# Kernel tuning notes

Measured on AMD Instinct MI355X. Metric: run time of the kernel, lower is better.

Reference implementation:

```python
import jax, jax.numpy as jnp
import numpy as np

N = 100000   # nodes
E = 1250000  # directed edges
F = 32       # node_features
H = 64       # hidden_channels
C = 10       # num_classes
NEG_SLOPE = 0.2  # GATConv default LeakyReLU slope


def _glorot(key, shape):
    fan_in = shape[0]
    return jax.random.normal(key, shape, jnp.float32) / np.sqrt(fan_in)


def setup_inputs() -> dict:
    k = jax.random.split(jax.random.key(0), 16)
    x = jax.random.normal(k[0], (N, F), jnp.float32)
    edge_index = jax.random.randint(k[1], (2, E), 0, N, dtype=jnp.int32)
    return {
        "x": x,
        "edge_index": edge_index,
        # GCNConv 1
        "W1": _glorot(k[2], (F, H)), "b1": jnp.zeros((H,), jnp.float32),
        # GATConv (heads=1)
        "W2": _glorot(k[3], (H, H)),
        "a_src": _glorot(k[4], (H,)), "a_dst": _glorot(k[5], (H,)),
        "b2": jnp.zeros((H,), jnp.float32),
        # GCNConv 3
        "W3": _glorot(k[6], (H, H)), "b3": jnp.zeros((H,), jnp.float32),
        # optimization head
        "Wopt": _glorot(k[7], (H, C)), "bopt": jnp.zeros((C,), jnp.float32),
        # bottleneck detector MLP
        "Wb1": _glorot(k[8], (H, 32)), "bb1": jnp.zeros((32,), jnp.float32),
        "Wb2": _glorot(k[9], (32, 1)), "bb2": jnp.zeros((1,), jnp.float32),
    }


def _gcn_conv(x, W, b, src, dst, n):
    # PyG GCNConv: self-loops already appended to src/dst by caller.
    h = x @ W  # [n, out]
    deg = jnp.zeros((n,), x.dtype).at[dst].add(1.0)
    dinv = jax.lax.rsqrt(jnp.maximum(deg, 1e-12))
    norm = dinv[src] * dinv[dst]  # [e]
    msg = h[src] * norm[:, None]  # gather + scale
    out = jnp.zeros_like(h).at[dst].add(msg)  # scatter-add
    return out + b


def _gat_conv(x, W, a_src, a_dst, b, src, dst, n):
    # PyG GATConv, heads=1: self-loops already appended.
    h = x @ W  # [n, out]
    alpha_s = h @ a_src  # [n]
    alpha_d = h @ a_dst  # [n]
    e = jax.nn.leaky_relu(alpha_s[src] + alpha_d[dst], NEG_SLOPE)  # [e]
    # softmax over incoming edges of each dst node
    emax = jax.ops.segment_max(e, dst, num_segments=n)
    p = jnp.exp(e - emax[dst])
    denom = jax.ops.segment_sum(p, dst, num_segments=n)
    alpha = p / denom[dst]
    out = jnp.zeros_like(h).at[dst].add(h[src] * alpha[:, None])
    return out + b


def reference(x, edge_index, W1, b1, W2, a_src, a_dst, b2, W3, b3,
              Wopt, bopt, Wb1, bb1, Wb2, bb2):
    n = x.shape[0]
    loops = jnp.arange(n, dtype=edge_index.dtype)
    src = jnp.concatenate([edge_index[0], loops])
    dst = jnp.concatenate([edge_index[1], loops])

    h = jax.nn.relu(_gcn_conv(x, W1, b1, src, dst, n))
    h = jax.nn.relu(_gat_conv(h, W2, a_src, a_dst, b2, src, dst, n))
    h = jax.nn.relu(_gcn_conv(h, W3, b3, src, dst, n))

    optimizations = h @ Wopt + bopt                     # [n, C]
    bottlenecks = jax.nn.sigmoid(jax.nn.relu(h @ Wb1 + bb1) @ Wb2 + bb2)  # [n, 1]
    graph_embedding = h.mean(axis=0)                    # [H]
    return optimizations, bottlenecks, graph_embedding
```

## Files before the change

### kernel.cpp

```cpp
#include <hip/hip_runtime.h>
#include <hip/hip_bf16.h>


#define CAP 64
#define NP2 128
#define NB2MAX 800

__device__ __forceinline__ int uwave(){
  return __builtin_amdgcn_readfirstlane(threadIdx.x >> 6);
}
__device__ __forceinline__ unsigned short f2bf(float f){
  unsigned u = __float_as_uint(f);
  return (unsigned short)((u + 0x7fffu + ((u >> 16) & 1u)) >> 16);
}
__device__ __forceinline__ float bfl(unsigned u){ return __uint_as_float(u << 16); }
__device__ __forceinline__ float bfh(unsigned u){ return __uint_as_float(u & 0xffff0000u); }
__device__ __forceinline__ float rdlane(float v, int l){
  return __uint_as_float(__builtin_amdgcn_readlane(__float_as_uint(v), l));
}

__global__ void k_setup(const float* __restrict__ Wopt, const float* __restrict__ bopt,
                        const float* __restrict__ Wb1, const float* __restrict__ bb1,
                        float* __restrict__ Wcat, float* __restrict__ bcat,
                        int* __restrict__ bcnt, unsigned short* __restrict__ tb,
                        unsigned short* __restrict__ xh, float* __restrict__ emb_acc,
                        int n, int nb2){
  int i = blockIdx.x*blockDim.x + threadIdx.x;
  if (i < nb2) bcnt[i] = 0;
  if (blockIdx.x == 0){
    int tid = threadIdx.x;
    for (int j = tid; j < 4096; j += 256){
      int f = j >> 6, c = j & 63;
      float w = 0.f;
      if (c < 10)       w = Wopt[f*10 + c];
      else if (c >= 32) w = Wb1[f*32 + (c-32)];
      Wcat[j] = w;
    }
    if (tid < 64){
      float b = 0.f;
      if (tid < 10)       b = bopt[tid];
      else if (tid >= 32) b = bb1[tid-32];
      bcat[tid] = b;
      tb[(size_t)n*64 + tid] = 0;
      emb_acc[tid] = 0.f;
    }
    if (tid >= 64 && tid < 96) xh[(size_t)n*32 + (tid-64)] = 0;
  }
}

__global__ __launch_bounds__(256) void k_part(const int* __restrict__ src,
                        const int* __restrict__ dst,
                        uint2* __restrict__ pairs, int* __restrict__ bcnt,
                        int e, int nb2, int pbcap){
  __shared__ int lcnt[NB2MAX];
  __shared__ int lbase[NB2MAX];
  int tid = threadIdx.x;
  for (int j = tid; j < nb2; j += 256) lcnt[j] = 0;
  __syncthreads();
  int i0 = blockIdx.x*2048 + tid*8;
  int d[8], s[8], bk[8], lp[8];
  int nv = e - i0;
  if (nv > 8) nv = 8;
  if (nv < 0) nv = 0;
  if (nv == 8){
    int4 d0 = *(const int4*)(dst + i0), d1 = *(const int4*)(dst + i0 + 4);
    int4 s0 = *(const int4*)(src + i0), s1 = *(const int4*)(src + i0 + 4);
    d[0]=d0.x; d[1]=d0.y; d[2]=d0.z; d[3]=d0.w;
    d[4]=d1.x; d[5]=d1.y; d[6]=d1.z; d[7]=d1.w;
    s[0]=s0.x; s[1]=s0.y; s[2]=s0.z; s[3]=s0.w;
    s[4]=s1.x; s[5]=s1.y; s[6]=s1.z; s[7]=s1.w;
  } else {
    #pragma unroll
    for (int j = 0; j < 8; j++){ d[j] = 0; s[j] = 0; }
    for (int j = 0; j < nv; j++){ d[j] = dst[i0+j]; s[j] = src[i0+j]; }
  }
  #pragma unroll
  for (int j = 0; j < 8; j++){
    if (j < nv){
      bk[j] = d[j] >> 7;
      lp[j] = atomicAdd(&lcnt[bk[j]], 1);
    }
  }
  __syncthreads();
  for (int j = tid; j < nb2; j += 256){
    int c = lcnt[j];
    if (c) lbase[j] = atomicAdd(&bcnt[j], c);
  }
  __syncthreads();
  #pragma unroll
  for (int j = 0; j < 8; j++){
    if (j < nv){
      int p = lbase[bk[j]] + lp[j];
      if (p < pbcap)
        pairs[(size_t)bk[j]*pbcap + p] = make_uint2((unsigned)d[j], (unsigned)s[j]);
    }
  }
}

__global__ __launch_bounds__(256) void k_fill(const uint2* __restrict__ pairs,
                        const int* __restrict__ bcnt, int* __restrict__ cnt,
                        int* __restrict__ adj, int pbcap, int n){
  __shared__ int lc[NP2];
  __shared__ int ladj[NP2*CAP];
  int b = blockIdx.x;
  int lo = b << 7;
  int nn = min(NP2, n - lo);
  int tid = threadIdx.x;
  for (int j = tid; j < NP2; j += 256) lc[j] = 0;
  __syncthreads();
  int m = bcnt[b];
  if (m > pbcap) m = pbcap;
  const uint2* pb = pairs + (size_t)b*pbcap;
  for (int j = tid; j < m; j += 256){
    uint2 p = pb[j];
    int r = (int)p.x - lo;
    int pos = atomicAdd(&lc[r], 1);
    if (pos < CAP) ladj[(r << 6) + pos] = (int)p.y;
  }
  __syncthreads();
  if (tid < nn) cnt[lo + tid] = lc[tid];
  int tot = nn << 4;
  uint4* ga = (uint4*)(adj + (size_t)lo*CAP);
  const uint4* la = (const uint4*)ladj;
  for (int j = tid; j < tot; j += 256) ga[j] = la[j];
}

__global__ void k_castscale(const float* __restrict__ x, const int* __restrict__ cnt,
                            unsigned short* __restrict__ xh, int total4){
  int i = blockIdx.x*blockDim.x + threadIdx.x;
  if (i >= total4) return;
  int row = i >> 3;
  float dv = rsqrtf((float)(cnt[row] + 1));
  float4 v = ((const float4*)x)[i];
  uint2 o;
  o.x = (unsigned)f2bf(v.x*dv) | ((unsigned)f2bf(v.y*dv) << 16);
  o.y = (unsigned)f2bf(v.z*dv) | ((unsigned)f2bf(v.w*dv) << 16);
  ((uint2*)xh)[i] = o;
}

__global__ __launch_bounds__(256) void k_agg32g(const unsigned short* __restrict__ xh,
                          const int* __restrict__ adj, const int* __restrict__ cnt,
                          const float* __restrict__ W1, const float* __restrict__ b1,
                          unsigned short* __restrict__ h, int n){
  int lane = threadIdx.x & 63;
  float wreg[32];
  #pragma unroll
  for (int k = 0; k < 32; k++) wreg[k] = W1[k*64 + lane];
  float br = b1[lane];
  int v0 = blockIdx.x*8 + uwave()*2;
  if (v0 >= n) return;
  int v1 = v0 + 1;
  bool has1 = v1 < n;
  if (!has1) v1 = v0;
  int cn0 = cnt[v0], cn1 = cnt[v1];
  int c0 = min(cn0, CAP), c1 = min(cn1, CAP);
  int ureg0 = n, ureg1 = n;
  if (lane < c0) ureg0 = (adj + (size_t)v0*CAP)[lane];
  if (lane < c1) ureg1 = (adj + (size_t)v1*CAP)[lane];
  int g = lane >> 3, q = lane & 7;
  float4 a0 = {0.f,0.f,0.f,0.f}, a1 = {0.f,0.f,0.f,0.f};
  int itm = (max(c0, c1) + 7) >> 3;
  #pragma unroll 2
  for (int jj = 0; jj < itm; jj++){
    int u0 = __shfl(ureg0, jj*8 + g);
    int u1 = __shfl(ureg1, jj*8 + g);
    uint2 r0 = ((const uint2*)(xh + (size_t)u0*32))[q];
    uint2 r1 = ((const uint2*)(xh + (size_t)u1*32))[q];
    a0.x += bfl(r0.x); a0.y += bfh(r0.x); a0.z += bfl(r0.y); a0.w += bfh(r0.y);
    a1.x += bfl(r1.x); a1.y += bfh(r1.x); a1.z += bfl(r1.y); a1.w += bfh(r1.y);
  }
  #pragma unroll
  for (int off = 8; off <= 32; off <<= 1){
    a0.x += __shfl_xor(a0.x, off); a0.y += __shfl_xor(a0.y, off);
    a0.z += __shfl_xor(a0.z, off); a0.w += __shfl_xor(a0.w, off);
    a1.x += __shfl_xor(a1.x, off); a1.y += __shfl_xor(a1.y, off);
    a1.z += __shfl_xor(a1.z, off); a1.w += __shfl_xor(a1.w, off);
  }
  uint2 s0 = ((const uint2*)(xh + (size_t)v0*32))[q];
  uint2 s1 = ((const uint2*)(xh + (size_t)v1*32))[q];
  a0.x += bfl(s0.x); a0.y += bfh(s0.x); a0.z += bfl(s0.y); a0.w += bfh(s0.y);
  a1.x += bfl(s1.x); a1.y += bfh(s1.x); a1.z += bfl(s1.y); a1.w += bfh(s1.y);
  float dv0 = rsqrtf((float)(cn0 + 1)), dv1 = rsqrtf((float)(cn1 + 1));
  a0.x *= dv0; a0.y *= dv0; a0.z *= dv0; a0.w *= dv0;
  a1.x *= dv1; a1.y *= dv1; a1.z *= dv1; a1.w *= dv1;
  float h0 = br, h1v = br;
  #pragma unroll
  for (int q2 = 0; q2 < 8; q2++){
    float w0x = rdlane(a0.x, q2), w1x = rdlane(a1.x, q2);
    float w0y = rdlane(a0.y, q2), w1y = rdlane(a1.y, q2);
    float w0z = rdlane(a0.z, q2), w1z = rdlane(a1.z, q2);
    float w0w = rdlane(a0.w, q2), w1w = rdlane(a1.w, q2);
    h0 = fmaf(w0x, wreg[q2*4+0], h0); h1v = fmaf(w1x, wreg[q2*4+0], h1v);
    h0 = fmaf(w0y, wreg[q2*4+1], h0); h1v = fmaf(w1y, wreg[q2*4+1], h1v);
    h0 = fmaf(w0z, wreg[q2*4+2], h0); h1v = fmaf(w1z, wreg[q2*4+2], h1v);
    h0 = fmaf(w0w, wreg[q2*4+3], h0); h1v = fmaf(w1w, wreg[q2*4+3], h1v);
  }
  h[(size_t)v0*64 + lane] = f2bf(fmaxf(h0, 0.f));
  if (has1) h[(size_t)v1*64 + lane] = f2bf(fmaxf(h1v, 0.f));
}

template<bool SCALE>
__global__ __launch_bounds__(256, 4) void k_gemm_b(const unsigned short* __restrict__ x,
                       const float* __restrict__ W, const int* __restrict__ cnt,
                       unsigned short* __restrict__ t, int n){
  int lane = threadIdx.x & 63;
  int gw = blockIdx.x*4 + uwave();
  int nw = gridDim.x*4;
  float wreg[64];
  #pragma unroll
  for (int k = 0; k < 64; k++) wreg[k] = W[k*64 + lane];
  for (int v = gw; v < n; v += nw){
    const uint4* xr = (const uint4*)(x + (size_t)v*64);
    float acc = 0.f;
    #pragma unroll
    for (int k8 = 0; k8 < 8; k8++){
      uint4 c = xr[k8];
      acc = fmaf(bfl(c.x), wreg[k8*8+0], acc);
      acc = fmaf(bfh(c.x), wreg[k8*8+1], acc);
      acc = fmaf(bfl(c.y), wreg[k8*8+2], acc);
      acc = fmaf(bfh(c.y), wreg[k8*8+3], acc);
      acc = fmaf(bfl(c.z), wreg[k8*8+4], acc);
      acc = fmaf(bfh(c.z), wreg[k8*8+5], acc);
      acc = fmaf(bfl(c.w), wreg[k8*8+6], acc);
      acc = fmaf(bfh(c.w), wreg[k8*8+7], acc);
    }
    if (SCALE) acc *= rsqrtf((float)(cnt[v] + 1));
    t[(size_t)v*64 + lane] = f2bf(acc);
  }
}

__global__ __launch_bounds__(256, 4) void k_gemm_alpha(const unsigned short* __restrict__ x,
                       const float* __restrict__ W,
                       const float* __restrict__ asrc, const float* __restrict__ adst,
                       unsigned short* __restrict__ t, float* __restrict__ als,
                       float* __restrict__ ald, int n){
  int lane = threadIdx.x & 63;
  int gw = blockIdx.x*4 + uwave();
  int nw = gridDim.x*4;
  float wreg[64];
  #pragma unroll
  for (int k = 0; k < 64; k++) wreg[k] = W[k*64 + lane];
  float asr = asrc[lane], adr = adst[lane];
  for (int v = gw; v < n; v += nw){
    const uint4* xr = (const uint4*)(x + (size_t)v*64);
    float acc = 0.f;
    #pragma unroll
    for (int k8 = 0; k8 < 8; k8++){
      uint4 c = xr[k8];
      acc = fmaf(bfl(c.x), wreg[k8*8+0], acc);
      acc = fmaf(bfh(c.x), wreg[k8*8+1], acc);
      acc = fmaf(bfl(c.y), wreg[k8*8+2], acc);
      acc = fmaf(bfh(c.y), wreg[k8*8+3], acc);
      acc = fmaf(bfl(c.z), wreg[k8*8+4], acc);
      acc = fmaf(bfh(c.z), wreg[k8*8+5], acc);
      acc = fmaf(bfl(c.w), wreg[k8*8+6], acc);
      acc = fmaf(bfh(c.w), wreg[k8*8+7], acc);
    }
    t[(size_t)v*64 + lane] = f2bf(acc);
    float s1 = acc * asr, s2 = acc * adr;
    #pragma unroll
    for (int off = 32; off; off >>= 1){
      s1 += __shfl_xor(s1, off);
      s2 += __shfl_xor(s2, off);
    }
    if (lane == 0){ als[v] = s1; ald[v] = s2; }
  }
}

__global__ __launch_bounds__(256) void k_gcn_agg(const unsigned short* __restrict__ t,
                          const int* __restrict__ adj, const int* __restrict__ cnt,
                          const float* __restrict__ b, unsigned short* __restrict__ h, int n){
  int lane = threadIdx.x & 63;
  int v0 = blockIdx.x*8 + uwave()*2;
  if (v0 >= n) return;
  int v1 = v0 + 1;
  bool has1 = v1 < n;
  if (!has1) v1 = v0;
  int cn0 = cnt[v0], cn1 = cnt[v1];
  int c0 = min(cn0, CAP), c1 = min(cn1, CAP);
  int ureg0 = n, ureg1 = n;
  if (lane < c0) ureg0 = (adj + (size_t)v0*CAP)[lane];
  if (lane < c1) ureg1 = (adj + (size_t)v1*CAP)[lane];
  int g = lane >> 3, q = lane & 7;
  float a0[8] = {0,0,0,0,0,0,0,0}, a1[8] = {0,0,0,0,0,0,0,0};
  int itm = (max(c0, c1) + 7) >> 3;
  #pragma unroll 2
  for (int jj = 0; jj < itm; jj++){
    int u0 = __shfl(ureg0, jj*8 + g);
    int u1 = __shfl(ureg1, jj*8 + g);
    uint4 r0 = ((const uint4*)(t + (size_t)u0*64))[q];
    uint4 r1 = ((const uint4*)(t + (size_t)u1*64))[q];
    a0[0] += bfl(r0.x); a0[1] += bfh(r0.x); a0[2] += bfl(r0.y); a0[3] += bfh(r0.y);
    a0[4] += bfl(r0.z); a0[5] += bfh(r0.z); a0[6] += bfl(r0.w); a0[7] += bfh(r0.w);
    a1[0] += bfl(r1.x); a1[1] += bfh(r1.x); a1[2] += bfl(r1.y); a1[3] += bfh(r1.y);
    a1[4] += bfl(r1.z); a1[5] += bfh(r1.z); a1[6] += bfl(r1.w); a1[7] += bfh(r1.w);
  }
  #pragma unroll
  for (int off = 8; off <= 32; off <<= 1){
    #pragma unroll
    for (int k = 0; k < 8; k++){
      a0[k] += __shfl_xor(a0[k], off);
      a1[k] += __shfl_xor(a1[k], off);
    }
  }
  uint4 s0 = ((const uint4*)(t + (size_t)v0*64))[q];
  uint4 s1 = ((const uint4*)(t + (size_t)v1*64))[q];
  a0[0] += bfl(s0.x); a0[1] += bfh(s0.x); a0[2] += bfl(s0.y); a0[3] += bfh(s0.y);
  a0[4] += bfl(s0.z); a0[5] += bfh(s0.z); a0[6] += bfl(s0.w); a0[7] += bfh(s0.w);
  a1[0] += bfl(s1.x); a1[1] += bfh(s1.x); a1[2] += bfl(s1.y); a1[3] += bfh(s1.y);
  a1[4] += bfl(s1.z); a1[5] += bfh(s1.z); a1[6] += bfl(s1.w); a1[7] += bfh(s1.w);
  float dv0 = rsqrtf((float)(cn0 + 1)), dv1 = rsqrtf((float)(cn1 + 1));
  float4 b0 = ((const float4*)b)[2*q], b1v = ((const float4*)b)[2*q+1];
  if (g == 0){
    float r0 = fmaxf(fmaf(a0[0], dv0, b0.x), 0.f),  r1 = fmaxf(fmaf(a0[1], dv0, b0.y), 0.f);
    float r2 = fmaxf(fmaf(a0[2], dv0, b0.z), 0.f),  r3 = fmaxf(fmaf(a0[3], dv0, b0.w), 0.f);
    float r4 = fmaxf(fmaf(a0[4], dv0, b1v.x), 0.f), r5 = fmaxf(fmaf(a0[5], dv0, b1v.y), 0.f);
    float r6 = fmaxf(fmaf(a0[6], dv0, b1v.z), 0.f), r7 = fmaxf(fmaf(a0[7], dv0, b1v.w), 0.f);
    uint4 o;
    o.x = (unsigned)f2bf(r0) | ((unsigned)f2bf(r1) << 16);
    o.y = (unsigned)f2bf(r2) | ((unsigned)f2bf(r3) << 16);
    o.z = (unsigned)f2bf(r4) | ((unsigned)f2bf(r5) << 16);
    o.w = (unsigned)f2bf(r6) | ((unsigned)f2bf(r7) << 16);
    ((uint4*)(h + (size_t)v0*64))[q] = o;
  } else if (g == 1 && has1){
    float r0 = fmaxf(fmaf(a1[0], dv1, b0.x), 0.f),  r1 = fmaxf(fmaf(a1[1], dv1, b0.y), 0.f);
    float r2 = fmaxf(fmaf(a1[2], dv1, b0.z), 0.f),  r3 = fmaxf(fmaf(a1[3], dv1, b0.w), 0.f);
    float r4 = fmaxf(fmaf(a1[4], dv1, b1v.x), 0.f), r5 = fmaxf(fmaf(a1[5], dv1, b1v.y), 0.f);
    float r6 = fmaxf(fmaf(a1[6], dv1, b1v.z), 0.f), r7 = fmaxf(fmaf(a1[7], dv1, b1v.w), 0.f);
    uint4 o;
    o.x = (unsigned)f2bf(r0) | ((unsigned)f2bf(r1) << 16);
    o.y = (unsigned)f2bf(r2) | ((unsigned)f2bf(r3) << 16);
    o.z = (unsigned)f2bf(r4) | ((unsigned)f2bf(r5) << 16);
    o.w = (unsigned)f2bf(r6) | ((unsigned)f2bf(r7) << 16);
    ((uint4*)(h + (size_t)v1*64))[q] = o;
  }
}

__global__ __launch_bounds__(256) void k_gat_agg(const unsigned short* __restrict__ t,
                          const int* __restrict__ adj, const int* __restrict__ cnt,
                          const float* __restrict__ als, const float* __restrict__ ald,
                          const float* __restrict__ b, unsigned short* __restrict__ h, int n){
  int lane = threadIdx.x & 63;
  int v0 = blockIdx.x*8 + uwave()*2;
  if (v0 >= n) return;
  int v1 = v0 + 1;
  bool has1 = v1 < n;
  if (!has1) v1 = v0;
  int c0 = min(cnt[v0], CAP), c1 = min(cnt[v1], CAP);
  int ureg0 = n, ureg1 = n;
  if (lane < c0) ureg0 = (adj + (size_t)v0*CAP)[lane];
  if (lane < c1) ureg1 = (adj + (size_t)v1*CAP)[lane];
  int us0 = (lane < c0) ? ureg0 : v0;
  int us1 = (lane < c1) ? ureg1 : v1;
  float adv0 = ald[v0], adv1 = ald[v1];
  float e0 = als[us0] + adv0;
  float e1 = als[us1] + adv1;
  e0 = e0 > 0.f ? e0 : 0.2f*e0;
  e1 = e1 > 0.f ? e1 : 0.2f*e1;
  float es0 = als[v0] + adv0; es0 = es0 > 0.f ? es0 : 0.2f*es0;
  float es1 = als[v1] + adv1; es1 = es1 > 0.f ? es1 : 0.2f*es1;
  float em0 = (lane < c0) ? e0 : -1e30f;
  float em1 = (lane < c1) ? e1 : -1e30f;
  #pragma unroll
  for (int off = 32; off; off >>= 1){
    em0 = fmaxf(em0, __shfl_xor(em0, off));
    em1 = fmaxf(em1, __shfl_xor(em1, off));
  }
  em0 = fmaxf(em0, es0); em1 = fmaxf(em1, es1);
  float p0 = (lane < c0) ? __expf(e0 - em0) : 0.f;
  float p1 = (lane < c1) ? __expf(e1 - em1) : 0.f;
  float sm0 = p0, sm1 = p1;
  #pragma unroll
  for (int off = 32; off; off >>= 1){
    sm0 += __shfl_xor(sm0, off);
    sm1 += __shfl_xor(sm1, off);
  }
  float ps0 = __expf(es0 - em0), ps1 = __expf(es1 - em1);
  float inv0 = 1.f / (sm0 + ps0), inv1 = 1.f / (sm1 + ps1);
  int g = lane >> 3, q = lane & 7;
  float a0[8] = {0,0,0,0,0,0,0,0}, a1[8] = {0,0,0,0,0,0,0,0};
  int itm = (max(c0, c1) + 7) >> 3;
  #pragma unroll 2
  for (int jj = 0; jj < itm; jj++){
    int   u0 = __shfl(ureg0, jj*8 + g);
    int   u1 = __shfl(ureg1, jj*8 + g);
    float w0 = __shfl(p0,    jj*8 + g);
    float w1 = __shfl(p1,    jj*8 + g);
    uint4 r0 = ((const uint4*)(t + (size_t)u0*64))[q];
    uint4 r1 = ((const uint4*)(t + (size_t)u1*64))[q];
    a0[0] = fmaf(w0, bfl(r0.x), a0[0]); a0[1] = fmaf(w0, bfh(r0.x), a0[1]);
    a0[2] = fmaf(w0, bfl(r0.y), a0[2]); a0[3] = fmaf(w0, bfh(r0.y), a0[3]);
    a0[4] = fmaf(w0, bfl(r0.z), a0[4]); a0[5] = fmaf(w0, bfh(r0.z), a0[5]);
    a0[6] = fmaf(w0, bfl(r0.w), a0[6]); a0[7] = fmaf(w0, bfh(r0.w), a0[7]);
    a1[0] = fmaf(w1, bfl(r1.x), a1[0]); a1[1] = fmaf(w1, bfh(r1.x), a1[1]);
    a1[2] = fmaf(w1, bfl(r1.y), a1[2]); a1[3] = fmaf(w1, bfh(r1.y), a1[3]);
    a1[4] = fmaf(w1, bfl(r1.z), a1[4]); a1[5] = fmaf(w1, bfh(r1.z), a1[5]);
    a1[6] = fmaf(w1, bfl(r1.w), a1[6]); a1[7] = fmaf(w1, bfh(r1.w), a1[7]);
  }
  #pragma unroll
  for (int off = 8; off <= 32; off <<= 1){
    #pragma unroll
    for (int k = 0; k < 8; k++){
      a0[k] += __shfl_xor(a0[k], off);
      a1[k] += __shfl_xor(a1[k], off);
    }
  }
  uint4 s0 = ((const uint4*)(t + (size_t)v0*64))[q];
  uint4 s1 = ((const uint4*)(t + (size_t)v1*64))[q];
  a0[0] = fmaf(ps0, bfl(s0.x), a0[0]); a0[1] = fmaf(ps0, bfh(s0.x), a0[1]);
  a0[2] = fmaf(ps0, bfl(s0.y), a0[2]); a0[3] = fmaf(ps0, bfh(s0.y), a0[3]);
  a0[4] = fmaf(ps0, bfl(s0.z), a0[4]); a0[5] = fmaf(ps0, bfh(s0.z), a0[5]);
  a0[6] = fmaf(ps0, bfl(s0.w), a0[6]); a0[7] = fmaf(ps0, bfh(s0.w), a0[7]);
  a1[0] = fmaf(ps1, bfl(s1.x), a1[0]); a1[1] = fmaf(ps1, bfh(s1.x), a1[1]);
  a1[2] = fmaf(ps1, bfl(s1.y), a1[2]); a1[3] = fmaf(ps1, bfh(s1.y), a1[3]);
  a1[4] = fmaf(ps1, bfl(s1.z), a1[4]); a1[5] = fmaf(ps1, bfh(s1.z), a1[5]);
  a1[6] = fmaf(ps1, bfl(s1.w), a1[6]); a1[7] = fmaf(ps1, bfh(s1.w), a1[7]);
  float4 b0 = ((const float4*)b)[2*q], b1v = ((const float4*)b)[2*q+1];
  if (g == 0){
    float r0 = fmaxf(fmaf(a0[0], inv0, b0.x), 0.f),  r1 = fmaxf(fmaf(a0[1], inv0, b0.y), 0.f);
    float r2 = fmaxf(fmaf(a0[2], inv0, b0.z), 0.f),  r3 = fmaxf(fmaf(a0[3], inv0, b0.w), 0.f);
    float r4 = fmaxf(fmaf(a0[4], inv0, b1v.x), 0.f), r5 = fmaxf(fmaf(a0[5], inv0, b1v.y), 0.f);
    float r6 = fmaxf(fmaf(a0[6], inv0, b1v.z), 0.f), r7 = fmaxf(fmaf(a0[7], inv0, b1v.w), 0.f);
    uint4 o;
    o.x = (unsigned)f2bf(r0) | ((unsigned)f2bf(r1) << 16);
    o.y = (unsigned)f2bf(r2) | ((unsigned)f2bf(r3) << 16);
    o.z = (unsigned)f2bf(r4) | ((unsigned)f2bf(r5) << 16);
    o.w = (unsigned)f2bf(r6) | ((unsigned)f2bf(r7) << 16);
    ((uint4*)(h + (size_t)v0*64))[q] = o;
  } else if (g == 1 && has1){
    float r0 = fmaxf(fmaf(a1[0], inv1, b0.x), 0.f),  r1 = fmaxf(fmaf(a1[1], inv1, b0.y), 0.f);
    float r2 = fmaxf(fmaf(a1[2], inv1, b0.z), 0.f),  r3 = fmaxf(fmaf(a1[3], inv1, b0.w), 0.f);
    float r4 = fmaxf(fmaf(a1[4], inv1, b1v.x), 0.f), r5 = fmaxf(fmaf(a1[5], inv1, b1v.y), 0.f);
    float r6 = fmaxf(fmaf(a1[6], inv1, b1v.z), 0.f), r7 = fmaxf(fmaf(a1[7], inv1, b1v.w), 0.f);
    uint4 o;
    o.x = (unsigned)f2bf(r0) | ((unsigned)f2bf(r1) << 16);
    o.y = (unsigned)f2bf(r2) | ((unsigned)f2bf(r3) << 16);
    o.z = (unsigned)f2bf(r4) | ((unsigned)f2bf(r5) << 16);
    o.w = (unsigned)f2bf(r6) | ((unsigned)f2bf(r7) << 16);
    ((uint4*)(h + (size_t)v1*64))[q] = o;
  }
}

__global__ __launch_bounds__(256, 4) void k_heads(const unsigned short* __restrict__ h,
                        const float* __restrict__ Wcat, const float* __restrict__ bcat,
                        const float* __restrict__ Wb2, const float* __restrict__ bb2,
                        float* __restrict__ out_opt, float* __restrict__ out_bot, int n){
  int lane = threadIdx.x & 63;
  int gw = blockIdx.x*4 + uwave();
  int nw = gridDim.x*4;
  float wreg[64];
  #pragma unroll
  for (int k = 0; k < 64; k++) wreg[k] = Wcat[k*64 + lane];
  float bcr  = bcat[lane];
  float wb2r = (lane >= 32) ? Wb2[lane-32] : 0.f;
  float bb2r = bb2[0];
  for (int v = gw; v < n; v += nw){
    const uint4* xr = (const uint4*)(h + (size_t)v*64);
    float acc = bcr;
    #pragma unroll
    for (int k8 = 0; k8 < 8; k8++){
      uint4 c = xr[k8];
      acc = fmaf(bfl(c.x), wreg[k8*8+0], acc);
      acc = fmaf(bfh(c.x), wreg[k8*8+1], acc);
      acc = fmaf(bfl(c.y), wreg[k8*8+2], acc);
      acc = fmaf(bfh(c.y), wreg[k8*8+3], acc);
      acc = fmaf(bfl(c.z), wreg[k8*8+4], acc);
      acc = fmaf(bfh(c.z), wreg[k8*8+5], acc);
      acc = fmaf(bfl(c.w), wreg[k8*8+6], acc);
      acc = fmaf(bfh(c.w), wreg[k8*8+7], acc);
    }
    if (lane < 10) out_opt[(size_t)v*10 + lane] = acc;
    float contrib = fmaxf(acc, 0.f) * wb2r;
    #pragma unroll
    for (int off = 32; off; off >>= 1) contrib += __shfl_xor(contrib, off);
    if (lane == 0) out_bot[v] = 1.f / (1.f + __expf(-(contrib + bb2r)));
  }
}

__global__ __launch_bounds__(256) void k_mean(const unsigned short* __restrict__ h,
                       float* __restrict__ emb_acc, int n){
  __shared__ float red[256];
  int tid = threadIdx.x;
  int w = tid >> 6, lane = tid & 63;
  float s = 0.f;
  for (int r = blockIdx.x*4 + w; r < n; r += 1024)
    s += __uint_as_float(((unsigned)h[(size_t)r*64 + lane]) << 16);
  red[tid] = s;
  __syncthreads();
  if (tid < 64)
    atomicAdd(&emb_acc[tid], red[tid] + red[64+tid] + red[128+tid] + red[192+tid]);
}

__global__ void k_embed(const float* __restrict__ emb_acc, float* __restrict__ out_emb,
                        float invn){
  if (threadIdx.x < 64) out_emb[threadIdx.x] = emb_acc[threadIdx.x] * invn;
}

extern "C" void kernel_launch(void* const* d_in, const int* in_sizes, int n_in,
                              void* d_out, int out_size, void* d_ws, size_t ws_size,
                              hipStream_t stream) {
  const float* x    = (const float*)d_in[0];
  const int*   ei   = (const int*)d_in[1];
  const float* W1   = (const float*)d_in[2];
  const float* b1   = (const float*)d_in[3];
  const float* W2   = (const float*)d_in[4];
  const float* a_s  = (const float*)d_in[5];
  const float* a_d  = (const float*)d_in[6];
  const float* b2   = (const float*)d_in[7];
  const float* W3   = (const float*)d_in[8];
  const float* b3   = (const float*)d_in[9];
  const float* Wopt = (const float*)d_in[10];
  const float* bopt = (const float*)d_in[11];
  const float* Wb1  = (const float*)d_in[12];
  const float* bb1  = (const float*)d_in[13];
  const float* Wb2  = (const float*)d_in[14];
  const float* bb2  = (const float*)d_in[15];

  int n = in_sizes[0] / 32;
  int e = in_sizes[1] / 2;
  const int* src = ei;
  const int* dst = ei + e;

  char* ws = (char*)d_ws;
  size_t off = 0;
  auto alloc = [&](size_t bytes) -> void* {
    void* p = ws + off;
    off += (bytes + 255) & ~(size_t)255;
    return p;
  };
  int nb2 = (n + NP2 - 1) >> 7;
  int*            cnt     = (int*)           alloc((size_t)n * 4);
  int*            adj     = (int*)           alloc((size_t)n * CAP * 4);
  float*          als     = (float*)         alloc((size_t)n * 4);
  float*          ald     = (float*)         alloc((size_t)n * 4);
  unsigned short* xh      = (unsigned short*)alloc((size_t)(n+1) * 32 * 2);
  unsigned short* tb      = (unsigned short*)alloc((size_t)(n+1) * 64 * 2);
  unsigned short* hbuf    = (unsigned short*)alloc((size_t)n * 64 * 2);
  float*          emb_acc = (float*)         alloc((size_t)64 * 4);
  float*          Wcat    = (float*)         alloc((size_t)4096 * 4);
  float*          bcat    = (float*)         alloc((size_t)64 * 4);
  int*            bcnt    = (int*)           alloc((size_t)nb2 * 4);

  int pbcap = e / nb2 + 384;
  long pcap_max = ((long)n * 128) / ((long)nb2 * 8);
  if (pbcap > (int)pcap_max) pbcap = (int)pcap_max;
  uint2* pairs = (uint2*)hbuf;

  float* out_opt = (float*)d_out;
  float* out_bot = out_opt + (size_t)n * 10;
  float* out_emb = out_bot + n;

  int nb8    = (n + 7) / 8;
  int nbN    = (n + 255) / 256;
  int nbP    = (e + 2047) / 2048;
  int total4 = n*32/4;
  int nbC    = (total4 + 255) / 256;

  k_setup<<<nbN, 256, 0, stream>>>(Wopt, bopt, Wb1, bb1, Wcat, bcat,
                                   bcnt, tb, xh, emb_acc, n, nb2);
  k_part<<<nbP, 256, 0, stream>>>(src, dst, pairs, bcnt, e, nb2, pbcap);
  k_fill<<<nb2, 256, 0, stream>>>(pairs, bcnt, cnt, adj, pbcap, n);
  k_castscale<<<nbC, 256, 0, stream>>>(x, cnt, xh, total4);

  k_agg32g<<<nb8, 256, 0, stream>>>(xh, adj, cnt, W1, b1, hbuf, n);

  k_gemm_alpha<<<1024, 256, 0, stream>>>(hbuf, W2, a_s, a_d, tb, als, ald, n);
  k_gat_agg<<<nb8, 256, 0, stream>>>(tb, adj, cnt, als, ald, b2, hbuf, n);

  k_gemm_b<true><<<1024, 256, 0, stream>>>(hbuf, W3, cnt, tb, n);
  k_gcn_agg<<<nb8, 256, 0, stream>>>(tb, adj, cnt, b3, hbuf, n);

  k_heads<<<1024, 256, 0, stream>>>(hbuf, Wcat, bcat, Wb2, bb2,
                                    out_opt, out_bot, n);
  k_mean<<<256, 256, 0, stream>>>(hbuf, emb_acc, n);
  k_embed<<<1, 64, 0, stream>>>(emb_acc, out_emb, 1.0f / (float)n);
}
```

Baseline: 356.6 us.

## Switch GCN and GAT aggregation to one node per wave, one feature per lane

Both aggregation kernels are restructured so that each wavefront handles a single destination node, with each lane owning one of the 64 features. Neighbours are walked serially in an unroll-by-4 loop using scalar-style index loads. This removes the two-nodes-per-wave packing, the 8-way group split and the cross-lane shuffle reductions. In exchange, each gather issues a 2-byte load per lane (128 contiguous bytes per row) instead of 16-byte vector loads, the GAT kernel recomputes exp per edge in every lane, and the grid is doubled.

```diff
diff --git a/kernel.cpp b/kernel.cpp
--- a/kernel.cpp
+++ b/kernel.cpp
@@ -15,6 +15,7 @@
 }
 __device__ __forceinline__ float bfl(unsigned u){ return __uint_as_float(u << 16); }
 __device__ __forceinline__ float bfh(unsigned u){ return __uint_as_float(u & 0xffff0000u); }
+__device__ __forceinline__ float bfu(unsigned short s){ return __uint_as_float(((unsigned)s) << 16); }
 __device__ __forceinline__ float rdlane(float v, int l){
   return __uint_as_float(__builtin_amdgcn_readlane(__float_as_uint(v), l));
 }
@@ -271,69 +272,28 @@
                           const int* __restrict__ adj, const int* __restrict__ cnt,
                           const float* __restrict__ b, unsigned short* __restrict__ h, int n){
   int lane = threadIdx.x & 63;
-  int v0 = blockIdx.x*8 + uwave()*2;
-  if (v0 >= n) return;
-  int v1 = v0 + 1;
-  bool has1 = v1 < n;
-  if (!has1) v1 = v0;
-  int cn0 = cnt[v0], cn1 = cnt[v1];
-  int c0 = min(cn0, CAP), c1 = min(cn1, CAP);
-  int ureg0 = n, ureg1 = n;
-  if (lane < c0) ureg0 = (adj + (size_t)v0*CAP)[lane];
-  if (lane < c1) ureg1 = (adj + (size_t)v1*CAP)[lane];
-  int g = lane >> 3, q = lane & 7;
-  float a0[8] = {0,0,0,0,0,0,0,0}, a1[8] = {0,0,0,0,0,0,0,0};
-  int itm = (max(c0, c1) + 7) >> 3;
-  #pragma unroll 2
-  for (int jj = 0; jj < itm; jj++){
-    int u0 = __shfl(ureg0, jj*8 + g);
-    int u1 = __shfl(ureg1, jj*8 + g);
-    uint4 r0 = ((const uint4*)(t + (size_t)u0*64))[q];
-    uint4 r1 = ((const uint4*)(t + (size_t)u1*64))[q];
-    a0[0] += bfl(r0.x); a0[1] += bfh(r0.x); a0[2] += bfl(r0.y); a0[3] += bfh(r0.y);
-    a0[4] += bfl(r0.z); a0[5] += bfh(r0.z); a0[6] += bfl(r0.w); a0[7] += bfh(r0.w);
-    a1[0] += bfl(r1.x); a1[1] += bfh(r1.x); a1[2] += bfl(r1.y); a1[3] += bfh(r1.y);
-    a1[4] += bfl(r1.z); a1[5] += bfh(r1.z); a1[6] += bfl(r1.w); a1[7] += bfh(r1.w);
-  }
-  #pragma unroll
-  for (int off = 8; off <= 32; off <<= 1){
-    #pragma unroll
-    for (int k = 0; k < 8; k++){
-      a0[k] += __shfl_xor(a0[k], off);
-      a1[k] += __shfl_xor(a1[k], off);
-    }
-  }
-  uint4 s0 = ((const uint4*)(t + (size_t)v0*64))[q];
-  uint4 s1 = ((const uint4*)(t + (size_t)v1*64))[q];
-  a0[0] += bfl(s0.x); a0[1] += bfh(s0.x); a0[2] += bfl(s0.y); a0[3] += bfh(s0.y);
-  a0[4] += bfl(s0.z); a0[5] += bfh(s0.z); a0[6] += bfl(s0.w); a0[7] += bfh(s0.w);
-  a1[0] += bfl(s1.x); a1[1] += bfh(s1.x); a1[2] += bfl(s1.y); a1[3] += bfh(s1.y);
-  a1[4] += bfl(s1.z); a1[5] += bfh(s1.z); a1[6] += bfl(s1.w); a1[7] += bfh(s1.w);
-  float dv0 = rsqrtf((float)(cn0 + 1)), dv1 = rsqrtf((float)(cn1 + 1));
-  float4 b0 = ((const float4*)b)[2*q], b1v = ((const float4*)b)[2*q+1];
-  if (g == 0){
-    float r0 = fmaxf(fmaf(a0[0], dv0, b0.x), 0.f),  r1 = fmaxf(fmaf(a0[1], dv0, b0.y), 0.f);
-    float r2 = fmaxf(fmaf(a0[2], dv0, b0.z), 0.f),  r3 = fmaxf(fmaf(a0[3], dv0, b0.w), 0.f);
-    float r4 = fmaxf(fmaf(a0[4], dv0, b1v.x), 0.f), r5 = fmaxf(fmaf(a0[5], dv0, b1v.y), 0.f);
-    float r6 = fmaxf(fmaf(a0[6], dv0, b1v.z), 0.f), r7 = fmaxf(fmaf(a0[7], dv0, b1v.w), 0.f);
-    uint4 o;
-    o.x = (unsigned)f2bf(r0) | ((unsigned)f2bf(r1) << 16);
-    o.y = (unsigned)f2bf(r2) | ((unsigned)f2bf(r3) << 16);
-    o.z = (unsigned)f2bf(r4) | ((unsigned)f2bf(r5) << 16);
-    o.w = (unsigned)f2bf(r6) | ((unsigned)f2bf(r7) << 16);
-    ((uint4*)(h + (size_t)v0*64))[q] = o;
-  } else if (g == 1 && has1){
-    float r0 = fmaxf(fmaf(a1[0], dv1, b0.x), 0.f),  r1 = fmaxf(fmaf(a1[1], dv1, b0.y), 0.f);
-    float r2 = fmaxf(fmaf(a1[2], dv1, b0.z), 0.f),  r3 = fmaxf(fmaf(a1[3], dv1, b0.w), 0.f);
-    float r4 = fmaxf(fmaf(a1[4], dv1, b1v.x), 0.f), r5 = fmaxf(fmaf(a1[5], dv1, b1v.y), 0.f);
-    float r6 = fmaxf(fmaf(a1[6], dv1, b1v.z), 0.f), r7 = fmaxf(fmaf(a1[7], dv1, b1v.w), 0.f);
-    uint4 o;
-    o.x = (unsigned)f2bf(r0) | ((unsigned)f2bf(r1) << 16);
-    o.y = (unsigned)f2bf(r2) | ((unsigned)f2bf(r3) << 16);
-    o.z = (unsigned)f2bf(r4) | ((unsigned)f2bf(r5) << 16);
-    o.w = (unsigned)f2bf(r6) | ((unsigned)f2bf(r7) << 16);
-    ((uint4*)(h + (size_t)v1*64))[q] = o;
-  }
+  int v = blockIdx.x*4 + uwave();
+  if (v >= n) return;
+  int cn = cnt[v];
+  int c = min(cn, CAP);
+  const int* row = adj + (size_t)v*CAP;
+  float acc = bfu(t[(size_t)v*64 + lane]);
+  int j = 0;
+  for (; j + 3 < c; j += 4){
+    int u0 = row[j], u1 = row[j+1], u2 = row[j+2], u3 = row[j+3];
+    float x0 = bfu(t[(size_t)u0*64 + lane]);
+    float x1 = bfu(t[(size_t)u1*64 + lane]);
+    float x2 = bfu(t[(size_t)u2*64 + lane]);
+    float x3 = bfu(t[(size_t)u3*64 + lane]);
+    acc += x0; acc += x1; acc += x2; acc += x3;
+  }
+  for (; j < c; j++){
+    int u0 = row[j];
+    acc += bfu(t[(size_t)u0*64 + lane]);
+  }
+  float dv = rsqrtf((float)(cn + 1));
+  float out = fmaxf(fmaf(acc, dv, b[lane]), 0.f);
+  h[(size_t)v*64 + lane] = f2bf(out);
 }
 
 __global__ __launch_bounds__(256) void k_gat_agg(const unsigned short* __restrict__ t,
@@ -341,104 +301,53 @@
                           const float* __restrict__ als, const float* __restrict__ ald,
                           const float* __restrict__ b, unsigned short* __restrict__ h, int n){
   int lane = threadIdx.x & 63;
-  int v0 = blockIdx.x*8 + uwave()*2;
-  if (v0 >= n) return;
-  int v1 = v0 + 1;
-  bool has1 = v1 < n;
-  if (!has1) v1 = v0;
-  int c0 = min(cnt[v0], CAP), c1 = min(cnt[v1], CAP);
-  int ureg0 = n, ureg1 = n;
-  if (lane < c0) ureg0 = (adj + (size_t)v0*CAP)[lane];
-  if (lane < c1) ureg1 = (adj + (size_t)v1*CAP)[lane];
-  int us0 = (lane < c0) ? ureg0 : v0;
-  int us1 = (lane < c1) ? ureg1 : v1;
-  float adv0 = ald[v0], adv1 = ald[v1];
-  float e0 = als[us0] + adv0;
-  float e1 = als[us1] + adv1;
-  e0 = e0 > 0.f ? e0 : 0.2f*e0;
-  e1 = e1 > 0.f ? e1 : 0.2f*e1;
-  float es0 = als[v0] + adv0; es0 = es0 > 0.f ? es0 : 0.2f*es0;
-  float es1 = als[v1] + adv1; es1 = es1 > 0.f ? es1 : 0.2f*es1;
-  float em0 = (lane < c0) ? e0 : -1e30f;
-  float em1 = (lane < c1) ? e1 : -1e30f;
-  #pragma unroll
-  for (int off = 32; off; off >>= 1){
-    em0 = fmaxf(em0, __shfl_xor(em0, off));
-    em1 = fmaxf(em1, __shfl_xor(em1, off));
-  }
-  em0 = fmaxf(em0, es0); em1 = fmaxf(em1, es1);
-  float p0 = (lane < c0) ? __expf(e0 - em0) : 0.f;
-  float p1 = (lane < c1) ? __expf(e1 - em1) : 0.f;
-  float sm0 = p0, sm1 = p1;
-  #pragma unroll
-  for (int off = 32; off; off >>= 1){
-    sm0 += __shfl_xor(sm0, off);
-    sm1 += __shfl_xor(sm1, off);
-  }
-  float ps0 = __expf(es0 - em0), ps1 = __expf(es1 - em1);
-  float inv0 = 1.f / (sm0 + ps0), inv1 = 1.f / (sm1 + ps1);
-  int g = lane >> 3, q = lane & 7;
-  float a0[8] = {0,0,0,0,0,0,0,0}, a1[8] = {0,0,0,0,0,0,0,0};
-  int itm = (max(c0, c1) + 7) >> 3;
-  #pragma unroll 2
-  for (int jj = 0; jj < itm; jj++){
-    int   u0 = __shfl(ureg0, jj*8 + g);
-    int   u1 = __shfl(ureg1, jj*8 + g);
-    float w0 = __shfl(p0,    jj*8 + g);
-    float w1 = __shfl(p1,    jj*8 + g);
-    uint4 r0 = ((const uint4*)(t + (size_t)u0*64))[q];
-    uint4 r1 = ((const uint4*)(t + (size_t)u1*64))[q];
-    a0[0] = fmaf(w0, bfl(r0.x), a0[0]); a0[1] = fmaf(w0, bfh(r0.x), a0[1]);
-    a0[2] = fmaf(w0, bfl(r0.y), a0[2]); a0[3] = fmaf(w0, bfh(r0.y), a0[3]);
-    a0[4] = fmaf(w0, bfl(r0.z), a0[4]); a0[5] = fmaf(w0, bfh(r0.z), a0[5]);
-    a0[6] = fmaf(w0, bfl(r0.w), a0[6]); a0[7] = fmaf(w0, bfh(r0.w), a0[7]);
-    a1[0] = fmaf(w1, bfl(r1.x), a1[0]); a1[1] = fmaf(w1, bfh(r1.x), a1[1]);
-    a1[2] = fmaf(w1, bfl(r1.y), a1[2]); a1[3] = fmaf(w1, bfh(r1.y), a1[3]);
-    a1[4] = fmaf(w1, bfl(r1.z), a1[4]); a1[5] = fmaf(w1, bfh(r1.z), a1[5]);
-    a1[6] = fmaf(w1, bfl(r1.w), a1[6]); a1[7] = fmaf(w1, bfh(r1.w), a1[7]);
-  }
-  #pragma unroll
-  for (int off = 8; off <= 32; off <<= 1){
-    #pragma unroll
-    for (int k = 0; k < 8; k++){
-      a0[k] += __shfl_xor(a0[k], off);
-      a1[k] += __shfl_xor(a1[k], off);
-    }
-  }
-  uint4 s0 = ((const uint4*)(t + (size_t)v0*64))[q];
-  uint4 s1 = ((const uint4*)(t + (size_t)v1*64))[q];
-  a0[0] = fmaf(ps0, bfl(s0.x), a0[0]); a0[1] = fmaf(ps0, bfh(s0.x), a0[1]);
-  a0[2] = fmaf(ps0, bfl(s0.y), a0[2]); a0[3] = fmaf(ps0, bfh(s0.y), a0[3]);
-  a0[4] = fmaf(ps0, bfl(s0.z), a0[4]); a0[5] = fmaf(ps0, bfh(s0.z), a0[5]);
-  a0[6] = fmaf(ps0, bfl(s0.w), a0[6]); a0[7] = fmaf(ps0, bfh(s0.w), a0[7]);
-  a1[0] = fmaf(ps1, bfl(s1.x), a1[0]); a1[1] = fmaf(ps1, bfh(s1.x), a1[1]);
-  a1[2] = fmaf(ps1, bfl(s1.y), a1[2]); a1[3] = fmaf(ps1, bfh(s1.y), a1[3]);
-  a1[4] = fmaf(ps1, bfl(s1.z), a1[4]); a1[5] = fmaf(ps1, bfh(s1.z), a1[5]);
-  a1[6] = fmaf(ps1, bfl(s1.w), a1[6]); a1[7] = fmaf(ps1, bfh(s1.w), a1[7]);
-  float4 b0 = ((const float4*)b)[2*q], b1v = ((const float4*)b)[2*q+1];
-  if (g == 0){
-    float r0 = fmaxf(fmaf(a0[0], inv0, b0.x), 0.f),  r1 = fmaxf(fmaf(a0[1], inv0, b0.y), 0.f);
-    float r2 = fmaxf(fmaf(a0[2], inv0, b0.z), 0.f),  r3 = fmaxf(fmaf(a0[3], inv0, b0.w), 0.f);
-    float r4 = fmaxf(fmaf(a0[4], inv0, b1v.x), 0.f), r5 = fmaxf(fmaf(a0[5], inv0, b1v.y), 0.f);
-    float r6 = fmaxf(fmaf(a0[6], inv0, b1v.z), 0.f), r7 = fmaxf(fmaf(a0[7], inv0, b1v.w), 0.f);
-    uint4 o;
-    o.x = (unsigned)f2bf(r0) | ((unsigned)f2bf(r1) << 16);
-    o.y = (unsigned)f2bf(r2) | ((unsigned)f2bf(r3) << 16);
-    o.z = (unsigned)f2bf(r4) | ((unsigned)f2bf(r5) << 16);
-    o.w = (unsigned)f2bf(r6) | ((unsigned)f2bf(r7) << 16);
-    ((uint4*)(h + (size_t)v0*64))[q] = o;
-  } else if (g == 1 && has1){
-    float r0 = fmaxf(fmaf(a1[0], inv1, b0.x), 0.f),  r1 = fmaxf(fmaf(a1[1], inv1, b0.y), 0.f);
-    float r2 = fmaxf(fmaf(a1[2], inv1, b0.z), 0.f),  r3 = fmaxf(fmaf(a1[3], inv1, b0.w), 0.f);
-    float r4 = fmaxf(fmaf(a1[4], inv1, b1v.x), 0.f), r5 = fmaxf(fmaf(a1[5], inv1, b1v.y), 0.f);
-    float r6 = fmaxf(fmaf(a1[6], inv1, b1v.z), 0.f), r7 = fmaxf(fmaf(a1[7], inv1, b1v.w), 0.f);
-    uint4 o;
-    o.x = (unsigned)f2bf(r0) | ((unsigned)f2bf(r1) << 16);
-    o.y = (unsigned)f2bf(r2) | ((unsigned)f2bf(r3) << 16);
-    o.z = (unsigned)f2bf(r4) | ((unsigned)f2bf(r5) << 16);
-    o.w = (unsigned)f2bf(r6) | ((unsigned)f2bf(r7) << 16);
-    ((uint4*)(h + (size_t)v1*64))[q] = o;
-  }
+  int v = blockIdx.x*4 + uwave();
+  if (v >= n) return;
+  int c = min(cnt[v], CAP);
+  const int* row = adj + (size_t)v*CAP;
+  int ureg = v;
+  if (lane < c) ureg = row[lane];
+  float adv = ald[v];
+  float e = als[ureg] + adv;
+  e = e > 0.f ? e : 0.2f*e;
+  float es = als[v] + adv; es = es > 0.f ? es : 0.2f*es;
+  float em = (lane < c) ? e : -1e30f;
+  #pragma unroll
+  for (int off = 32; off; off >>= 1) em = fmaxf(em, __shfl_xor(em, off));
+  em = fmaxf(em, es);
+  float p = (lane < c) ? __expf(e - em) : 0.f;
+  float sm = p;
+  #pragma unroll
+  for (int off = 32; off; off >>= 1) sm += __shfl_xor(sm, off);
+  float ps = __expf(es - em);
+  float inv = 1.f / (sm + ps);
+  float acc = ps * bfu(t[(size_t)v*64 + lane]);
+  int j = 0;
+  for (; j + 3 < c; j += 4){
+    int u0 = row[j], u1 = row[j+1], u2 = row[j+2], u3 = row[j+3];
+    float a0 = als[u0], a1 = als[u1], a2 = als[u2], a3 = als[u3];
+    float x0 = bfu(t[(size_t)u0*64 + lane]);
+    float x1 = bfu(t[(size_t)u1*64 + lane]);
+    float x2 = bfu(t[(size_t)u2*64 + lane]);
+    float x3 = bfu(t[(size_t)u3*64 + lane]);
+    float e0 = a0 + adv; e0 = e0 > 0.f ? e0 : 0.2f*e0;
+    float e1 = a1 + adv; e1 = e1 > 0.f ? e1 : 0.2f*e1;
+    float e2 = a2 + adv; e2 = e2 > 0.f ? e2 : 0.2f*e2;
+    float e3 = a3 + adv; e3 = e3 > 0.f ? e3 : 0.2f*e3;
+    acc = fmaf(__expf(e0 - em), x0, acc);
+    acc = fmaf(__expf(e1 - em), x1, acc);
+    acc = fmaf(__expf(e2 - em), x2, acc);
+    acc = fmaf(__expf(e3 - em), x3, acc);
+  }
+  for (; j < c; j++){
+    int u0 = row[j];
+    float a0 = als[u0];
+    float x0 = bfu(t[(size_t)u0*64 + lane]);
+    float e0 = a0 + adv; e0 = e0 > 0.f ? e0 : 0.2f*e0;
+    acc = fmaf(__expf(e0 - em), x0, acc);
+  }
+  float out = fmaxf(fmaf(acc, inv, b[lane]), 0.f);
+  h[(size_t)v*64 + lane] = f2bf(out);
 }
 
 __global__ __launch_bounds__(256, 4) void k_heads(const unsigned short* __restrict__ h,
@@ -551,6 +460,7 @@
   float* out_emb = out_bot + n;
 
   int nb8    = (n + 7) / 8;
+  int nb4    = (n + 3) / 4;
   int nbN    = (n + 255) / 256;
   int nbP    = (e + 2047) / 2048;
   int total4 = n*32/4;
@@ -565,10 +475,10 @@
   k_agg32g<<<nb8, 256, 0, stream>>>(xh, adj, cnt, W1, b1, hbuf, n);
 
   k_gemm_alpha<<<1024, 256, 0, stream>>>(hbuf, W2, a_s, a_d, tb, als, ald, n);
-  k_gat_agg<<<nb8, 256, 0, stream>>>(tb, adj, cnt, als, ald, b2, hbuf, n);
+  k_gat_agg<<<nb4, 256, 0, stream>>>(tb, adj, cnt, als, ald, b2, hbuf, n);
 
   k_gemm_b<true><<<1024, 256, 0, stream>>>(hbuf, W3, cnt, tb, n);
-  k_gcn_agg<<<nb8, 256, 0, stream>>>(tb, adj, cnt, b3, hbuf, n);
+  k_gcn_agg<<<nb4, 256, 0, stream>>>(tb, adj, cnt, b3, hbuf, n);
 
   k_heads<<<1024, 256, 0, stream>>>(hbuf, Wcat, bcat, Wb2, bb2,
                                     out_opt, out_bot, n);
```

After: 375.1 us. 1.05x slower.
